# Kernel tuning notes

Hardware: AMD Instinct MI355X
Metric: run time of the kernel (lower is better)

Reference implementation:

```python
import jax, jax.numpy as jnp
import numpy as np
from jax import lax

B, T, L = 16, 256, 1024       # batch, seq_length, input_size
NF = 32                        # num_filters
KS = [3, 5, 7]                 # kernel_sizes
H = 1024                       # feature_size
GRU_IN = NF * len(KS)          # 96


def setup_inputs() -> dict:
    key = jax.random.key(0)
    ks = jax.random.split(key, 20)
    def rn(k, shape, scale):
        return (jax.random.normal(k, shape, dtype=jnp.float32) * scale)
    inp = {
        "x": jax.random.normal(ks[0], (B, T, L), dtype=jnp.float32),
        "conv_w3": rn(ks[1], (NF, 1, 3), (2.0 / 3) ** 0.5),
        "conv_b3": jnp.zeros((NF,), jnp.float32),
        "conv_w5": rn(ks[2], (NF, 1, 5), (2.0 / 5) ** 0.5),
        "conv_b5": jnp.zeros((NF,), jnp.float32),
        "conv_w7": rn(ks[3], (NF, 1, 7), (2.0 / 7) ** 0.5),
        "conv_b7": jnp.zeros((NF,), jnp.float32),
        "gru_w_ih": rn(ks[4], (3 * H, GRU_IN), GRU_IN ** -0.5),
        "gru_w_hh": rn(ks[5], (3 * H, H), H ** -0.5),
        "gru_b_ih": jnp.zeros((3 * H,), jnp.float32),
        "gru_b_hh": jnp.zeros((3 * H,), jnp.float32),
        "attn_w1": rn(ks[6], (H, H), H ** -0.5),
        "attn_b1": jnp.zeros((H,), jnp.float32),
        "attn_w2": rn(ks[7], (1, H), H ** -0.5),
        "attn_b2": jnp.zeros((1,), jnp.float32),
        "fi_w1": rn(ks[8], (H, H), H ** -0.5),
        "fi_b1": jnp.zeros((H,), jnp.float32),
        "fi_w2": rn(ks[9], (H, H), H ** -0.5),
        "fi_b2": jnp.zeros((H,), jnp.float32),
        "lateral": jnp.full((H, H), 0.1, jnp.float32),
    }
    return inp


def _forward(x, conv_w3, conv_b3, conv_w5, conv_b5, conv_w7, conv_b7,
             gru_w_ih, gru_w_hh, gru_b_ih, gru_b_hh,
             attn_w1, attn_b1, attn_w2, attn_b2,
             fi_w1, fi_b1, fi_w2, fi_b2, lateral):
    b, t, l = x.shape
    # --- per-timestep conv branches (no cross-time dependence -> vectorize over B*T) ---
    xt = x.reshape(b * t, 1, l)  # (BT, C=1, L)
    pooled = []
    for w, bias in ((conv_w3, conv_b3), (conv_w5, conv_b5), (conv_w7, conv_b7)):
        y = lax.conv_general_dilated(xt, w, (1,), "SAME",
                                     dimension_numbers=("NCH", "OIH", "NCH"))
        y = jax.nn.relu(y + bias[None, :, None])
        pooled.append(jnp.max(y, axis=-1))  # adaptive_max_pool1d -> (BT, NF)
    feat = jnp.concatenate(pooled, axis=1).reshape(b, t, -1)  # (B, T, 3*NF)

    # --- GRU over time (sequential carry) ---
    gates_x = jnp.einsum("bti,gi->btg", feat, gru_w_ih) + gru_b_ih  # (B,T,3H)

    def step(h, gx):
        gh = h @ gru_w_hh.T + gru_b_hh
        xr, xz, xn = jnp.split(gx, 3, axis=-1)
        hr, hz, hn = jnp.split(gh, 3, axis=-1)
        r = jax.nn.sigmoid(xr + hr)
        z = jax.nn.sigmoid(xz + hz)
        n = jnp.tanh(xn + r * hn)
        h_new = (1.0 - z) * n + z * h
        return h_new, h_new

    h0 = jnp.zeros((b, gru_w_hh.shape[1]), x.dtype)
    _, hs = lax.scan(step, h0, jnp.swapaxes(gates_x, 0, 1))  # (T,B,H)
    hs = jnp.swapaxes(hs, 0, 1)  # (B,T,H)

    # --- attention: per-step softmax over a length-1 axis -> weights are all 1 ---
    scores = jnp.tanh(hs @ attn_w1.T + attn_b1) @ attn_w2.T + attn_b2  # (B,T,1)
    attn = jax.nn.softmax(scores, axis=-1)  # softmax over singleton seq dim -> ones
    attended = hs * attn  # (B,T,H)

    # --- lateral inhibition + feature integration MLP ---
    inhib = attended - jax.nn.relu(jnp.einsum("bth,hf->btf", attended, lateral))
    features = jax.nn.relu(inhib @ fi_w1.T + fi_b1) @ fi_w2.T + fi_b2  # (B,T,H)
    return features, attn[..., 0]  # attention_weights (B,T)


def reference(x, conv_w3, conv_b3, conv_w5, conv_b5, conv_w7, conv_b7,
              gru_w_ih, gru_w_hh, gru_b_ih, gru_b_hh,
              attn_w1, attn_b1, attn_w2, attn_b2,
              fi_w1, fi_b1, fi_w2, fi_b2, lateral):
    return _forward(x, conv_w3, conv_b3, conv_w5, conv_b5, conv_w7, conv_b7,
                    gru_w_ih, gru_w_hh, gru_b_ih, gru_b_hh,
                    attn_w1, attn_b1, attn_w2, attn_b2,
                    fi_w1, fi_b1, fi_w2, fi_b2, lateral)
```

## Files before the change

### kernel.cpp

```cpp
#include <hip/hip_runtime.h>
#include <stdint.h>
#include <stddef.h>

#define B_   16
#define T_   256
#define L_   1024
#define H_   1024
#define G3_  3072
#define KIN_ 96
#define CONVB_ 4096

#define SENT_     0x7FC1
#define SENT_X2_  0x7FC17FC1u

typedef __attribute__((ext_vector_type(8))) __bf16 bf16x8;
typedef __attribute__((ext_vector_type(4))) float  f32x4;
typedef __attribute__((ext_vector_type(4))) int    i32x4;

static __device__ __forceinline__ unsigned short f2bf(float x) {
  unsigned int u = __builtin_bit_cast(unsigned int, x);
  u += 0x7FFFu + ((u >> 16) & 1u);
  return (unsigned short)(u >> 16);
}
static __device__ __forceinline__ float bf2f(unsigned short s) {
  unsigned int u = ((unsigned int)s) << 16;
  return __builtin_bit_cast(float, u);
}
static __device__ __forceinline__ unsigned sentmask(unsigned d) {
  const unsigned x = d ^ SENT_X2_;
  return (x - 0x00010001u) & ~x & 0x80008000u;
}

__global__ __launch_bounds__(256) void prep_conv_kernel(
    const float* __restrict__ x,
    const float* __restrict__ w3, const float* __restrict__ b3,
    const float* __restrict__ w5, const float* __restrict__ b5,
    const float* __restrict__ w7, const float* __restrict__ b7,
    unsigned short* __restrict__ feat,
    const float* __restrict__ whh,  unsigned short* __restrict__ whh_bf,
    const float* __restrict__ wih,  unsigned short* __restrict__ wih_bf,
    const float* __restrict__ fiw1, unsigned short* __restrict__ fiw1_bf,
    const float* __restrict__ fiw2, unsigned short* __restrict__ fiw2_bf,
    const float* __restrict__ lat,  unsigned short* __restrict__ latT_bf,
    unsigned short* __restrict__ hsbuf, float* __restrict__ attn_out) {
  __shared__ float xpad[L_ + 8];
  __shared__ float wlds[96][8];
  __shared__ float blds[96];
  __shared__ float wmax[4][96];
  const int tid = threadIdx.x;

  if (blockIdx.x >= CONVB_) {
    const int N0 = G3_ * H_;
    const int N1 = N0 + G3_ * KIN_;
    const int N2 = N1 + H_ * H_;
    const int N3 = N2 + H_ * H_;
    const int N4 = N3 + H_ * H_;
    const int N5 = N4 + T_ * B_ * H_ / 2;
    const int N6 = N5 + B_ * H_ / 2;
    const int N7 = N6 + B_ * T_;
    int i = (blockIdx.x - CONVB_) * 256 + tid;
    const int stride = (gridDim.x - CONVB_) * 256;
    unsigned int* hs32 = (unsigned int*)hsbuf;
    for (; i < N7; i += stride) {
      if (i < N0)      whh_bf[i] = f2bf(whh[i]);
      else if (i < N1) { const int j = i - N0; wih_bf[j]  = f2bf(wih[j]); }
      else if (i < N2) { const int j = i - N1; fiw1_bf[j] = f2bf(fiw1[j]); }
      else if (i < N3) { const int j = i - N2; fiw2_bf[j] = f2bf(fiw2[j]); }
      else if (i < N4) { const int j = i - N3; const int r = j >> 10, c = j & 1023;
                         latT_bf[(size_t)c * H_ + r] = f2bf(lat[j]); }
      else if (i < N5) { hs32[B_ * H_ / 2 + (i - N4)] = SENT_X2_; }
      else if (i < N6) { hs32[i - N5] = 0u; }
      else             { attn_out[i - N6] = 1.0f; }
    }
    return;
  }

  const int rid = blockIdx.x;
  const int b = rid >> 8;
  const int t = rid & 255;
  const float* xr = x + (size_t)rid * L_;
  for (int off = tid; off < L_; off += 256) xpad[off + 3] = xr[off];
  if (tid < 3) xpad[tid] = 0.f;
  if (tid >= 3 && tid < 8) xpad[L_ + tid] = 0.f;
  if (tid < 96) {
    const int f = tid;
    float wv[8];
#pragma unroll
    for (int k = 0; k < 8; ++k) wv[k] = 0.f;
    float bv;
    if (f < 32)      { for (int k = 0; k < 3; ++k) wv[k + 2] = w3[f * 3 + k]; bv = b3[f]; }
    else if (f < 64) { int ff = f - 32; for (int k = 0; k < 5; ++k) wv[k + 1] = w5[ff * 5 + k]; bv = b5[ff]; }
    else             { int ff = f - 64; for (int k = 0; k < 7; ++k) wv[k] = w7[ff * 7 + k]; bv = b7[ff]; }
#pragma unroll
    for (int k = 0; k < 8; ++k) wlds[f][k] = wv[k];
    blds[f] = bv;
  }
  __syncthreads();
  const int w = tid >> 6, lane = tid & 63;
  const int p0 = w * 256 + lane * 4;
  float xv[10];
#pragma unroll
  for (int i = 0; i < 10; ++i) xv[i] = xpad[p0 + i];
  for (int f = 0; f < 96; ++f) {
    float a0 = 0.f, a1 = 0.f, a2 = 0.f, a3 = 0.f;
#pragma unroll
    for (int k = 0; k < 7; ++k) {
      const float wk = wlds[f][k];
      a0 = fmaf(wk, xv[k],     a0);
      a1 = fmaf(wk, xv[k + 1], a1);
      a2 = fmaf(wk, xv[k + 2], a2);
      a3 = fmaf(wk, xv[k + 3], a3);
    }
    float m = fmaxf(fmaxf(a0, a1), fmaxf(a2, a3));
#pragma unroll
    for (int d = 1; d < 64; d <<= 1) m = fmaxf(m, __shfl_xor(m, d, 64));
    if (lane == 0) wmax[w][f] = m;
  }
  __syncthreads();
  if (tid < 96) {
    float m = fmaxf(fmaxf(wmax[0][tid], wmax[1][tid]),
                    fmaxf(wmax[2][tid], wmax[3][tid]));
    m += blds[tid];
    m = m > 0.f ? m : 0.f;
    feat[(size_t)(t * B_ + b) * KIN_ + tid] = f2bf(m);
  }
}

template <int EP>
__global__ __launch_bounds__(256) void gemm_kernel(
    const unsigned short* __restrict__ A,
    const unsigned short* __restrict__ Bm,
    int M, int N, int K, int lda, int ldb,
    const float* __restrict__ bias,
    float* __restrict__ outF,
    unsigned short* __restrict__ outB) {
  __shared__ __align__(16) unsigned short As[2][128 * 40];
  __shared__ __align__(16) unsigned short Bs[2][128 * 40];
  const int tid = threadIdx.x;
  const int n0 = blockIdx.x * 128;
  const int m0 = blockIdx.y * 128;
  const int w = tid >> 6;
  const int l = tid & 63;
  const int lr = l & 15;
  const int lk = (l >> 4) * 8;
  const int srow = tid >> 2;
  const int skc = (tid & 3) * 8;

  f32x4 acc[2][8];
#pragma unroll
  for (int i = 0; i < 2; ++i)
#pragma unroll
    for (int j = 0; j < 8; ++j) acc[i][j] = (f32x4){0.f, 0.f, 0.f, 0.f};

  const int NK = K >> 5;
  const unsigned short* Aptr  = A  + (size_t)(m0 + srow)      * lda + skc;
  const unsigned short* Aptr2 = A  + (size_t)(m0 + 64 + srow) * lda + skc;
  const unsigned short* Bptr  = Bm + (size_t)(n0 + srow)      * ldb + skc;
  const unsigned short* Bptr2 = Bm + (size_t)(n0 + 64 + srow) * ldb + skc;

  i32x4 ar0 = *(const i32x4*)(Aptr);
  i32x4 ar1 = *(const i32x4*)(Aptr2);
  i32x4 br0 = *(const i32x4*)(Bptr);
  i32x4 br1 = *(const i32x4*)(Bptr2);
  *(i32x4*)&As[0][srow * 40 + skc]        = ar0;
  *(i32x4*)&As[0][(64 + srow) * 40 + skc] = ar1;
  *(i32x4*)&Bs[0][srow * 40 + skc]        = br0;
  *(i32x4*)&Bs[0][(64 + srow) * 40 + skc] = br1;
  __syncthreads();

  for (int kk = 0; kk < NK; ++kk) {
    const int cur = kk & 1;
    if (kk + 1 < NK) {
      const int ko = (kk + 1) << 5;
      ar0 = *(const i32x4*)(Aptr  + ko);
      ar1 = *(const i32x4*)(Aptr2 + ko);
      br0 = *(const i32x4*)(Bptr  + ko);
      br1 = *(const i32x4*)(Bptr2 + ko);
    }
    const bf16x8 a0 = *(const bf16x8*)&As[cur][(w * 32 + lr) * 40 + lk];
    const bf16x8 a1 = *(const bf16x8*)&As[cur][(w * 32 + 16 + lr) * 40 + lk];
#pragma unroll
    for (int nt = 0; nt < 8; ++nt) {
      const bf16x8 bb = *(const bf16x8*)&Bs[cur][(nt * 16 + lr) * 40 + lk];
      acc[0][nt] = __builtin_amdgcn_mfma_f32_16x16x32_bf16(a0, bb, acc[0][nt], 0, 0, 0);
      acc[1][nt] = __builtin_amdgcn_mfma_f32_16x16x32_bf16(a1, bb, acc[1][nt], 0, 0, 0);
    }
    __syncthreads();
    if (kk + 1 < NK) {
      const int nxt = cur ^ 1;
      *(i32x4*)&As[nxt][srow * 40 + skc]        = ar0;
      *(i32x4*)&As[nxt][(64 + srow) * 40 + skc] = ar1;
      *(i32x4*)&Bs[nxt][srow * 40 + skc]        = br0;
      *(i32x4*)&Bs[nxt][(64 + srow) * 40 + skc] = br1;
    }
    __syncthreads();
  }

#pragma unroll
  for (int mt = 0; mt < 2; ++mt) {
#pragma unroll
    for (int nt = 0; nt < 8; ++nt) {
      const f32x4 v = acc[mt][nt];
      const int gcol = n0 + nt * 16 + lr;
#pragma unroll
      for (int e = 0; e < 4; ++e) {
        const int grow = m0 + w * 32 + mt * 16 + (l >> 4) * 4 + e;
        const float val = v[e];
        if (EP == 0) {
          outF[(size_t)grow * N + gcol] = val + bias[gcol];
        } else if (EP == 1) {
          const float hsv = bf2f(A[(size_t)grow * lda + gcol]);
          outB[(size_t)grow * N + gcol] = f2bf(hsv - fmaxf(val, 0.f));
        } else if (EP == 2) {
          outB[(size_t)grow * N + gcol] = f2bf(fmaxf(val + bias[gcol], 0.f));
        } else {
          const int tt = grow >> 4;
          const int bb2 = grow & 15;
          outF[((size_t)bb2 * T_ + tt) * H_ + gcol] = val + bias[gcol];
        }
      }
    }
  }
}

__global__ __launch_bounds__(512, 1) void gru_scan_kernel(
    const unsigned short* __restrict__ Whh,
    const float* __restrict__ gates,
    const float* __restrict__ bhh,
    unsigned short* __restrict__ hs) {
  const int g = blockIdx.x;
  const int tid = threadIdx.x;

  __shared__ float ghp[8][3][16][36];
  const int w = tid >> 6;
  const int l = tid & 63;
  const int lr = l & 15;
  const int lk8 = (l >> 4) * 8;
  const int j0 = g * 32;

  const unsigned short* a00 = Whh + (size_t)(0 * H_ + j0 +      lr) * H_ + w * 128 + lk8;
  const unsigned short* a01 = Whh + (size_t)(0 * H_ + j0 + 16 + lr) * H_ + w * 128 + lk8;
  const unsigned short* a10 = Whh + (size_t)(1 * H_ + j0 +      lr) * H_ + w * 128 + lk8;
  const unsigned short* a11 = Whh + (size_t)(1 * H_ + j0 + 16 + lr) * H_ + w * 128 + lk8;
  const unsigned short* a20 = Whh + (size_t)(2 * H_ + j0 +      lr) * H_ + w * 128 + lk8;
  const unsigned short* a21 = Whh + (size_t)(2 * H_ + j0 + 16 + lr) * H_ + w * 128 + lk8;
  i32x4 q0, q1, q2, q3, q4, q5, q6, q7, q8, q9, q10, q11,
        q12, q13, q14, q15, q16, q17, q18, q19, q20, q21, q22, q23;
  asm volatile(
      "global_load_dwordx4 %0,  %24, off\n\t"
      "global_load_dwordx4 %1,  %24, off offset:64\n\t"
      "global_load_dwordx4 %2,  %24, off offset:128\n\t"
      "global_load_dwordx4 %3,  %24, off offset:192\n\t"
      "global_load_dwordx4 %4,  %25, off\n\t"
      "global_load_dwordx4 %5,  %25, off offset:64\n\t"
      "global_load_dwordx4 %6,  %25, off offset:128\n\t"
      "global_load_dwordx4 %7,  %25, off offset:192\n\t"
      "global_load_dwordx4 %8,  %26, off\n\t"
      "global_load_dwordx4 %9,  %26, off offset:64\n\t"
      "global_load_dwordx4 %10, %26, off offset:128\n\t"
      "global_load_dwordx4 %11, %26, off offset:192\n\t"
      "global_load_dwordx4 %12, %27, off\n\t"
      "global_load_dwordx4 %13, %27, off offset:64\n\t"
      "global_load_dwordx4 %14, %27, off offset:128\n\t"
      "global_load_dwordx4 %15, %27, off offset:192\n\t"
      "global_load_dwordx4 %16, %28, off\n\t"
      "global_load_dwordx4 %17, %28, off offset:64\n\t"
      "global_load_dwordx4 %18, %28, off offset:128\n\t"
      "global_load_dwordx4 %19, %28, off offset:192\n\t"
      "global_load_dwordx4 %20, %29, off\n\t"
      "global_load_dwordx4 %21, %29, off offset:64\n\t"
      "global_load_dwordx4 %22, %29, off offset:128\n\t"
      "global_load_dwordx4 %23, %29, off offset:192\n\t"
      "s_waitcnt vmcnt(0)"
      : "=&v"(q0), "=&v"(q1), "=&v"(q2), "=&v"(q3),
        "=&v"(q4), "=&v"(q5), "=&v"(q6), "=&v"(q7),
        "=&v"(q8), "=&v"(q9), "=&v"(q10), "=&v"(q11),
        "=&v"(q12), "=&v"(q13), "=&v"(q14), "=&v"(q15),
        "=&v"(q16), "=&v"(q17), "=&v"(q18), "=&v"(q19),
        "=&v"(q20), "=&v"(q21), "=&v"(q22), "=&v"(q23)
      : "v"(a00), "v"(a01), "v"(a10), "v"(a11), "v"(a20), "v"(a21));
  bf16x8 wf[24];
  wf[0]  = __builtin_bit_cast(bf16x8, q0);  wf[1]  = __builtin_bit_cast(bf16x8, q1);
  wf[2]  = __builtin_bit_cast(bf16x8, q2);  wf[3]  = __builtin_bit_cast(bf16x8, q3);
  wf[4]  = __builtin_bit_cast(bf16x8, q4);  wf[5]  = __builtin_bit_cast(bf16x8, q5);
  wf[6]  = __builtin_bit_cast(bf16x8, q6);  wf[7]  = __builtin_bit_cast(bf16x8, q7);
  wf[8]  = __builtin_bit_cast(bf16x8, q8);  wf[9]  = __builtin_bit_cast(bf16x8, q9);
  wf[10] = __builtin_bit_cast(bf16x8, q10); wf[11] = __builtin_bit_cast(bf16x8, q11);
  wf[12] = __builtin_bit_cast(bf16x8, q12); wf[13] = __builtin_bit_cast(bf16x8, q13);
  wf[14] = __builtin_bit_cast(bf16x8, q14); wf[15] = __builtin_bit_cast(bf16x8, q15);
  wf[16] = __builtin_bit_cast(bf16x8, q16); wf[17] = __builtin_bit_cast(bf16x8, q17);
  wf[18] = __builtin_bit_cast(bf16x8, q18); wf[19] = __builtin_bit_cast(bf16x8, q19);
  wf[20] = __builtin_bit_cast(bf16x8, q20); wf[21] = __builtin_bit_cast(bf16x8, q21);
  wf[22] = __builtin_bit_cast(bf16x8, q22); wf[23] = __builtin_bit_cast(bf16x8, q23);

  const int jb = tid & 31;
  const int bb = tid >> 5;
  const float bhr = bhh[j0 + jb];
  const float bhz = bhh[H_ + j0 + jb];
  const float bhn = bhh[2 * H_ + j0 + jb];
  float hprev = 0.f;

  for (int t = 0; t < T_; ++t) {
    const size_t grow = ((size_t)t * B_ + bb) * G3_;
    const float gxr = gates[grow + j0 + jb];
    const float gxz = gates[grow + H_ + j0 + jb];
    const float gxn = gates[grow + 2 * H_ + j0 + jb];

    const unsigned short* hp = hs + (size_t)t * (B_ * H_) +
                               (size_t)lr * H_ + w * 128 + lk8;
    i32x4 u0, u1, u2, u3;
    while (true) {
      asm volatile(
          "global_load_dwordx4 %0, %4, off sc0 sc1\n\t"
          "global_load_dwordx4 %1, %4, off offset:64 sc0 sc1\n\t"
          "global_load_dwordx4 %2, %4, off offset:128 sc0 sc1\n\t"
          "global_load_dwordx4 %3, %4, off offset:192 sc0 sc1\n\t"
          "s_waitcnt vmcnt(0)"
          : "=&v"(u0), "=&v"(u1), "=&v"(u2), "=&v"(u3)
          : "v"(hp)
          : "memory");
      const unsigned bad = sentmask(u0[0]) | sentmask(u0[3]) |
                           sentmask(u1[0]) | sentmask(u1[3]) |
                           sentmask(u2[0]) | sentmask(u2[3]) |
                           sentmask(u3[0]) | sentmask(u3[3]);
      if (__ballot(bad == 0) == ~0ull) break;
    }
    const bf16x8 hf0 = __builtin_bit_cast(bf16x8, u0);
    const bf16x8 hf1 = __builtin_bit_cast(bf16x8, u1);
    const bf16x8 hf2 = __builtin_bit_cast(bf16x8, u2);
    const bf16x8 hf3 = __builtin_bit_cast(bf16x8, u3);

    f32x4 C[3][2];
#pragma unroll
    for (int m = 0; m < 3; ++m)
#pragma unroll
      for (int ct = 0; ct < 2; ++ct) C[m][ct] = (f32x4){0.f, 0.f, 0.f, 0.f};
#pragma unroll
    for (int m = 0; m < 3; ++m)
#pragma unroll
      for (int ct = 0; ct < 2; ++ct) {
        C[m][ct] = __builtin_amdgcn_mfma_f32_16x16x32_bf16(wf[(m * 2 + ct) * 4 + 0], hf0, C[m][ct], 0, 0, 0);
        C[m][ct] = __builtin_amdgcn_mfma_f32_16x16x32_bf16(wf[(m * 2 + ct) * 4 + 1], hf1, C[m][ct], 0, 0, 0);
        C[m][ct] = __builtin_amdgcn_mfma_f32_16x16x32_bf16(wf[(m * 2 + ct) * 4 + 2], hf2, C[m][ct], 0, 0, 0);
        C[m][ct] = __builtin_amdgcn_mfma_f32_16x16x32_bf16(wf[(m * 2 + ct) * 4 + 3], hf3, C[m][ct], 0, 0, 0);
      }

    const int rb = (l >> 4) * 4;
#pragma unroll
    for (int m = 0; m < 3; ++m)
#pragma unroll
      for (int ct = 0; ct < 2; ++ct)
#pragma unroll
        for (int e = 0; e < 4; ++e)
          ghp[w][m][lr][ct * 16 + rb + e] = C[m][ct][e];
    __syncthreads();

    float hr = bhr, hz = bhz, hn = bhn;
#pragma unroll
    for (int w2 = 0; w2 < 8; ++w2) {
      hr += ghp[w2][0][bb][jb];
      hz += ghp[w2][1][bb][jb];
      hn += ghp[w2][2][bb][jb];
    }
    const float r = 1.f / (1.f + __expf(-(gxr + hr)));
    const float z = 1.f / (1.f + __expf(-(gxz + hz)));
    const float xn = gxn + r * hn;
    const float n = 2.f / (1.f + __expf(-2.f * xn)) - 1.f;
    const float hnew = (1.f - z) * n + z * hprev;
    hprev = hnew;

    const unsigned hv = (unsigned)f2bf(hnew);
    const int base = l & ~7;
    const unsigned s0 = __shfl(hv, base + 0, 64);
    const unsigned s1 = __shfl(hv, base + 1, 64);
    const unsigned s2 = __shfl(hv, base + 2, 64);
    const unsigned s3 = __shfl(hv, base + 3, 64);
    const unsigned s4 = __shfl(hv, base + 4, 64);
    const unsigned s5 = __shfl(hv, base + 5, 64);
    const unsigned s6 = __shfl(hv, base + 6, 64);
    const unsigned s7 = __shfl(hv, base + 7, 64);
    i32x4 pk;
    pk[0] = (int)(s0 | (s1 << 16));
    pk[1] = (int)(s2 | (s3 << 16));
    pk[2] = (int)(s4 | (s5 << 16));
    pk[3] = (int)(s6 | (s7 << 16));
    if ((l & 7) == 0) {
      unsigned short* sp = hs + ((size_t)(t + 1) * B_ + bb) * H_ + j0 + jb;
      asm volatile("global_store_dwordx4 %0, %1, off sc0 sc1"
                   :: "v"(sp), "v"(pk) : "memory");
    }
    __syncthreads();
  }
}

extern "C" void kernel_launch(void* const* d_in, const int* in_sizes, int n_in,
                              void* d_out, int out_size, void* d_ws, size_t ws_size,
                              hipStream_t stream) {
  (void)in_sizes; (void)n_in; (void)out_size; (void)ws_size;
  const float* x    = (const float*)d_in[0];
  const float* w3   = (const float*)d_in[1];
  const float* b3   = (const float*)d_in[2];
  const float* w5   = (const float*)d_in[3];
  const float* b5   = (const float*)d_in[4];
  const float* w7   = (const float*)d_in[5];
  const float* b7   = (const float*)d_in[6];
  const float* wih  = (const float*)d_in[7];
  const float* whh  = (const float*)d_in[8];
  const float* bih  = (const float*)d_in[9];
  const float* bhh  = (const float*)d_in[10];
  const float* fiw1 = (const float*)d_in[15];
  const float* fib1 = (const float*)d_in[16];
  const float* fiw2 = (const float*)d_in[17];
  const float* fib2 = (const float*)d_in[18];
  const float* lat  = (const float*)d_in[19];

  char* ws = (char*)d_ws;
  size_t off = 0;
  auto alloc = [&](size_t bytes) -> void* {
    void* p = ws + off;
    off += (bytes + 255) & ~(size_t)255;
    return p;
  };
  unsigned short* whh_bf  = (unsigned short*)alloc((size_t)G3_ * H_ * 2);
  unsigned short* wih_bf  = (unsigned short*)alloc((size_t)G3_ * KIN_ * 2);
  unsigned short* latT_bf = (unsigned short*)alloc((size_t)H_ * H_ * 2);
  unsigned short* fiw1_bf = (unsigned short*)alloc((size_t)H_ * H_ * 2);
  unsigned short* fiw2_bf = (unsigned short*)alloc((size_t)H_ * H_ * 2);
  unsigned short* feat_bf = (unsigned short*)alloc((size_t)B_ * T_ * KIN_ * 2);
  float*          gates   = (float*)alloc((size_t)B_ * T_ * G3_ * 4);
  unsigned short* hsbuf   = (unsigned short*)alloc((size_t)(T_ + 1) * B_ * H_ * 2);
  unsigned short* inhib   = (unsigned short*)alloc((size_t)B_ * T_ * H_ * 2);
  unsigned short* y1      = (unsigned short*)alloc((size_t)B_ * T_ * H_ * 2);

  prep_conv_kernel<<<CONVB_ + 2048, 256, 0, stream>>>(
      x, w3, b3, w5, b5, w7, b7, feat_bf,
      whh, whh_bf, wih, wih_bf, fiw1, fiw1_bf, fiw2, fiw2_bf,
      lat, latT_bf, hsbuf, (float*)d_out + (size_t)B_ * T_ * H_);

  {
    dim3 grid(G3_ / 128, (B_ * T_) / 128);
    gemm_kernel<0><<<grid, 256, 0, stream>>>(feat_bf, wih_bf, B_ * T_, G3_, KIN_,
                                             KIN_, KIN_, bih, gates, nullptr);
  }

  gru_scan_kernel<<<32, 512, 0, stream>>>(whh_bf, gates, bhh, hsbuf);

  const unsigned short* hs1 = hsbuf + (size_t)B_ * H_;
  {
    dim3 grid(H_ / 128, (B_ * T_) / 128);
    gemm_kernel<1><<<grid, 256, 0, stream>>>(hs1, latT_bf, B_ * T_, H_, H_,
                                             H_, H_, nullptr, nullptr, inhib);
    gemm_kernel<2><<<grid, 256, 0, stream>>>(inhib, fiw1_bf, B_ * T_, H_, H_,
                                             H_, H_, fib1, nullptr, y1);
    gemm_kernel<3><<<grid, 256, 0, stream>>>(y1, fiw2_bf, B_ * T_, H_, H_,
                                             H_, H_, fib2, (float*)d_out, nullptr);
  }
}
```

Baseline: 907.4 us.

## Halve GRU scan grid by giving each block 64 hidden columns

The persistent GRU scan kernel now launches 16 blocks instead of 32, with each block holding register-resident W_hh slices for 64 hidden units (two 32-column halves) and issuing twice as many MFMAs per step. The aim is to cut the number of blocks that must see each other's hidden-state writes every timestep, which reduces cross-block polling and synchronization latency per step. The cost is double the per-block matrix work and register pressure (48 bf16x8 weight fragments), plus a larger dynamically sized LDS reduction buffer with padded stride 69.

```diff
diff --git a/kernel.cpp b/kernel.cpp
--- a/kernel.cpp
+++ b/kernel.cpp
@@ -228,83 +228,112 @@
     const float* __restrict__ gates,
     const float* __restrict__ bhh,
     unsigned short* __restrict__ hs) {
+  extern __shared__ float ghp[];
   const int g = blockIdx.x;
   const int tid = threadIdx.x;
 
-  __shared__ float ghp[8][3][16][36];
   const int w = tid >> 6;
   const int l = tid & 63;
   const int lr = l & 15;
   const int lk8 = (l >> 4) * 8;
-  const int j0 = g * 32;
-
-  const unsigned short* a00 = Whh + (size_t)(0 * H_ + j0 +      lr) * H_ + w * 128 + lk8;
-  const unsigned short* a01 = Whh + (size_t)(0 * H_ + j0 + 16 + lr) * H_ + w * 128 + lk8;
-  const unsigned short* a10 = Whh + (size_t)(1 * H_ + j0 +      lr) * H_ + w * 128 + lk8;
-  const unsigned short* a11 = Whh + (size_t)(1 * H_ + j0 + 16 + lr) * H_ + w * 128 + lk8;
-  const unsigned short* a20 = Whh + (size_t)(2 * H_ + j0 +      lr) * H_ + w * 128 + lk8;
-  const unsigned short* a21 = Whh + (size_t)(2 * H_ + j0 + 16 + lr) * H_ + w * 128 + lk8;
-  i32x4 q0, q1, q2, q3, q4, q5, q6, q7, q8, q9, q10, q11,
-        q12, q13, q14, q15, q16, q17, q18, q19, q20, q21, q22, q23;
-  asm volatile(
-      "global_load_dwordx4 %0,  %24, off\n\t"
-      "global_load_dwordx4 %1,  %24, off offset:64\n\t"
-      "global_load_dwordx4 %2,  %24, off offset:128\n\t"
-      "global_load_dwordx4 %3,  %24, off offset:192\n\t"
-      "global_load_dwordx4 %4,  %25, off\n\t"
-      "global_load_dwordx4 %5,  %25, off offset:64\n\t"
-      "global_load_dwordx4 %6,  %25, off offset:128\n\t"
-      "global_load_dwordx4 %7,  %25, off offset:192\n\t"
-      "global_load_dwordx4 %8,  %26, off\n\t"
-      "global_load_dwordx4 %9,  %26, off offset:64\n\t"
-      "global_load_dwordx4 %10, %26, off offset:128\n\t"
-      "global_load_dwordx4 %11, %26, off offset:192\n\t"
-      "global_load_dwordx4 %12, %27, off\n\t"
-      "global_load_dwordx4 %13, %27, off offset:64\n\t"
-      "global_load_dwordx4 %14, %27, off offset:128\n\t"
-      "global_load_dwordx4 %15, %27, off offset:192\n\t"
-      "global_load_dwordx4 %16, %28, off\n\t"
-      "global_load_dwordx4 %17, %28, off offset:64\n\t"
-      "global_load_dwordx4 %18, %28, off offset:128\n\t"
-      "global_load_dwordx4 %19, %28, off offset:192\n\t"
-      "global_load_dwordx4 %20, %29, off\n\t"
-      "global_load_dwordx4 %21, %29, off offset:64\n\t"
-      "global_load_dwordx4 %22, %29, off offset:128\n\t"
-      "global_load_dwordx4 %23, %29, off offset:192\n\t"
-      "s_waitcnt vmcnt(0)"
-      : "=&v"(q0), "=&v"(q1), "=&v"(q2), "=&v"(q3),
-        "=&v"(q4), "=&v"(q5), "=&v"(q6), "=&v"(q7),
-        "=&v"(q8), "=&v"(q9), "=&v"(q10), "=&v"(q11),
-        "=&v"(q12), "=&v"(q13), "=&v"(q14), "=&v"(q15),
-        "=&v"(q16), "=&v"(q17), "=&v"(q18), "=&v"(q19),
-        "=&v"(q20), "=&v"(q21), "=&v"(q22), "=&v"(q23)
-      : "v"(a00), "v"(a01), "v"(a10), "v"(a11), "v"(a20), "v"(a21));
-  bf16x8 wf[24];
-  wf[0]  = __builtin_bit_cast(bf16x8, q0);  wf[1]  = __builtin_bit_cast(bf16x8, q1);
-  wf[2]  = __builtin_bit_cast(bf16x8, q2);  wf[3]  = __builtin_bit_cast(bf16x8, q3);
-  wf[4]  = __builtin_bit_cast(bf16x8, q4);  wf[5]  = __builtin_bit_cast(bf16x8, q5);
-  wf[6]  = __builtin_bit_cast(bf16x8, q6);  wf[7]  = __builtin_bit_cast(bf16x8, q7);
-  wf[8]  = __builtin_bit_cast(bf16x8, q8);  wf[9]  = __builtin_bit_cast(bf16x8, q9);
-  wf[10] = __builtin_bit_cast(bf16x8, q10); wf[11] = __builtin_bit_cast(bf16x8, q11);
-  wf[12] = __builtin_bit_cast(bf16x8, q12); wf[13] = __builtin_bit_cast(bf16x8, q13);
-  wf[14] = __builtin_bit_cast(bf16x8, q14); wf[15] = __builtin_bit_cast(bf16x8, q15);
-  wf[16] = __builtin_bit_cast(bf16x8, q16); wf[17] = __builtin_bit_cast(bf16x8, q17);
-  wf[18] = __builtin_bit_cast(bf16x8, q18); wf[19] = __builtin_bit_cast(bf16x8, q19);
-  wf[20] = __builtin_bit_cast(bf16x8, q20); wf[21] = __builtin_bit_cast(bf16x8, q21);
-  wf[22] = __builtin_bit_cast(bf16x8, q22); wf[23] = __builtin_bit_cast(bf16x8, q23);
+  const int j0 = g * 64;
+
+#define GHP(W, M, BB, CC) ghp[(((W) * 3 + (M)) * 16 + (BB)) * 69 + (CC)]
+
+  bf16x8 wf[48];
+#pragma unroll
+  for (int half = 0; half < 2; ++half) {
+    const int jh = j0 + half * 32;
+    const unsigned short* a00 = Whh + (size_t)(0 * H_ + jh +      lr) * H_ + w * 128 + lk8;
+    const unsigned short* a01 = Whh + (size_t)(0 * H_ + jh + 16 + lr) * H_ + w * 128 + lk8;
+    const unsigned short* a10 = Whh + (size_t)(1 * H_ + jh +      lr) * H_ + w * 128 + lk8;
+    const unsigned short* a11 = Whh + (size_t)(1 * H_ + jh + 16 + lr) * H_ + w * 128 + lk8;
+    const unsigned short* a20 = Whh + (size_t)(2 * H_ + jh +      lr) * H_ + w * 128 + lk8;
+    const unsigned short* a21 = Whh + (size_t)(2 * H_ + jh + 16 + lr) * H_ + w * 128 + lk8;
+    i32x4 q0, q1, q2, q3, q4, q5, q6, q7, q8, q9, q10, q11,
+          q12, q13, q14, q15, q16, q17, q18, q19, q20, q21, q22, q23;
+    asm volatile(
+        "global_load_dwordx4 %0,  %24, off\n\t"
+        "global_load_dwordx4 %1,  %24, off offset:64\n\t"
+        "global_load_dwordx4 %2,  %24, off offset:128\n\t"
+        "global_load_dwordx4 %3,  %24, off offset:192\n\t"
+        "global_load_dwordx4 %4,  %25, off\n\t"
+        "global_load_dwordx4 %5,  %25, off offset:64\n\t"
+        "global_load_dwordx4 %6,  %25, off offset:128\n\t"
+        "global_load_dwordx4 %7,  %25, off offset:192\n\t"
+        "global_load_dwordx4 %8,  %26, off\n\t"
+        "global_load_dwordx4 %9,  %26, off offset:64\n\t"
+        "global_load_dwordx4 %10, %26, off offset:128\n\t"
+        "global_load_dwordx4 %11, %26, off offset:192\n\t"
+        "global_load_dwordx4 %12, %27, off\n\t"
+        "global_load_dwordx4 %13, %27, off offset:64\n\t"
+        "global_load_dwordx4 %14, %27, off offset:128\n\t"
+        "global_load_dwordx4 %15, %27, off offset:192\n\t"
+        "global_load_dwordx4 %16, %28, off\n\t"
+        "global_load_dwordx4 %17, %28, off offset:64\n\t"
+        "global_load_dwordx4 %18, %28, off offset:128\n\t"
+        "global_load_dwordx4 %19, %28, off offset:192\n\t"
+        "global_load_dwordx4 %20, %29, off\n\t"
+        "global_load_dwordx4 %21, %29, off offset:64\n\t"
+        "global_load_dwordx4 %22, %29, off offset:128\n\t"
+        "global_load_dwordx4 %23, %29, off offset:192\n\t"
+        "s_waitcnt vmcnt(0)"
+        : "=&v"(q0), "=&v"(q1), "=&v"(q2), "=&v"(q3),
+          "=&v"(q4), "=&v"(q5), "=&v"(q6), "=&v"(q7),
+          "=&v"(q8), "=&v"(q9), "=&v"(q10), "=&v"(q11),
+          "=&v"(q12), "=&v"(q13), "=&v"(q14), "=&v"(q15),
+          "=&v"(q16), "=&v"(q17), "=&v"(q18), "=&v"(q19),
+          "=&v"(q20), "=&v"(q21), "=&v"(q22), "=&v"(q23)
+        : "v"(a00), "v"(a01), "v"(a10), "v"(a11), "v"(a20), "v"(a21));
+    const int b0 = half * 2;
+    wf[(0 * 4 + b0 + 0) * 4 + 0] = __builtin_bit_cast(bf16x8, q0);
+    wf[(0 * 4 + b0 + 0) * 4 + 1] = __builtin_bit_cast(bf16x8, q1);
+    wf[(0 * 4 + b0 + 0) * 4 + 2] = __builtin_bit_cast(bf16x8, q2);
+    wf[(0 * 4 + b0 + 0) * 4 + 3] = __builtin_bit_cast(bf16x8, q3);
+    wf[(0 * 4 + b0 + 1) * 4 + 0] = __builtin_bit_cast(bf16x8, q4);
+    wf[(0 * 4 + b0 + 1) * 4 + 1] = __builtin_bit_cast(bf16x8, q5);
+    wf[(0 * 4 + b0 + 1) * 4 + 2] = __builtin_bit_cast(bf16x8, q6);
+    wf[(0 * 4 + b0 + 1) * 4 + 3] = __builtin_bit_cast(bf16x8, q7);
+    wf[(1 * 4 + b0 + 0) * 4 + 0] = __builtin_bit_cast(bf16x8, q8);
+    wf[(1 * 4 + b0 + 0) * 4 + 1] = __builtin_bit_cast(bf16x8, q9);
+    wf[(1 * 4 + b0 + 0) * 4 + 2] = __builtin_bit_cast(bf16x8, q10);
+    wf[(1 * 4 + b0 + 0) * 4 + 3] = __builtin_bit_cast(bf16x8, q11);
+    wf[(1 * 4 + b0 + 1) * 4 + 0] = __builtin_bit_cast(bf16x8, q12);
+    wf[(1 * 4 + b0 + 1) * 4 + 1] = __builtin_bit_cast(bf16x8, q13);
+    wf[(1 * 4 + b0 + 1) * 4 + 2] = __builtin_bit_cast(bf16x8, q14);
+    wf[(1 * 4 + b0 + 1) * 4 + 3] = __builtin_bit_cast(bf16x8, q15);
+    wf[(2 * 4 + b0 + 0) * 4 + 0] = __builtin_bit_cast(bf16x8, q16);
+    wf[(2 * 4 + b0 + 0) * 4 + 1] = __builtin_bit_cast(bf16x8, q17);
+    wf[(2 * 4 + b0 + 0) * 4 + 2] = __builtin_bit_cast(bf16x8, q18);
+    wf[(2 * 4 + b0 + 0) * 4 + 3] = __builtin_bit_cast(bf16x8, q19);
+    wf[(2 * 4 + b0 + 1) * 4 + 0] = __builtin_bit_cast(bf16x8, q20);
+    wf[(2 * 4 + b0 + 1) * 4 + 1] = __builtin_bit_cast(bf16x8, q21);
+    wf[(2 * 4 + b0 + 1) * 4 + 2] = __builtin_bit_cast(bf16x8, q22);
+    wf[(2 * 4 + b0 + 1) * 4 + 3] = __builtin_bit_cast(bf16x8, q23);
+  }
 
   const int jb = tid & 31;
   const int bb = tid >> 5;
-  const float bhr = bhh[j0 + jb];
-  const float bhz = bhh[H_ + j0 + jb];
-  const float bhn = bhh[2 * H_ + j0 + jb];
-  float hprev = 0.f;
+  float bhg[2][3], hprev[2];
+#pragma unroll
+  for (int half = 0; half < 2; ++half) {
+    const int jc = j0 + half * 32 + jb;
+    bhg[half][0] = bhh[jc];
+    bhg[half][1] = bhh[H_ + jc];
+    bhg[half][2] = bhh[2 * H_ + jc];
+    hprev[half] = 0.f;
+  }
 
   for (int t = 0; t < T_; ++t) {
     const size_t grow = ((size_t)t * B_ + bb) * G3_;
-    const float gxr = gates[grow + j0 + jb];
-    const float gxz = gates[grow + H_ + j0 + jb];
-    const float gxn = gates[grow + 2 * H_ + j0 + jb];
+    float gx[2][3];
+#pragma unroll
+    for (int half = 0; half < 2; ++half) {
+      const int jc = j0 + half * 32 + jb;
+      gx[half][0] = gates[grow + jc];
+      gx[half][1] = gates[grow + H_ + jc];
+      gx[half][2] = gates[grow + 2 * H_ + jc];
+    }
 
     const unsigned short* hp = hs + (size_t)t * (B_ * H_) +
                                (size_t)lr * H_ + w * 128 + lk8;
@@ -330,67 +359,73 @@
     const bf16x8 hf2 = __builtin_bit_cast(bf16x8, u2);
     const bf16x8 hf3 = __builtin_bit_cast(bf16x8, u3);
 
-    f32x4 C[3][2];
+    f32x4 C[3][4];
 #pragma unroll
     for (int m = 0; m < 3; ++m)
 #pragma unroll
-      for (int ct = 0; ct < 2; ++ct) C[m][ct] = (f32x4){0.f, 0.f, 0.f, 0.f};
+      for (int ct = 0; ct < 4; ++ct) C[m][ct] = (f32x4){0.f, 0.f, 0.f, 0.f};
 #pragma unroll
     for (int m = 0; m < 3; ++m)
 #pragma unroll
-      for (int ct = 0; ct < 2; ++ct) {
-        C[m][ct] = __builtin_amdgcn_mfma_f32_16x16x32_bf16(wf[(m * 2 + ct) * 4 + 0], hf0, C[m][ct], 0, 0, 0);
-        C[m][ct] = __builtin_amdgcn_mfma_f32_16x16x32_bf16(wf[(m * 2 + ct) * 4 + 1], hf1, C[m][ct], 0, 0, 0);
-        C[m][ct] = __builtin_amdgcn_mfma_f32_16x16x32_bf16(wf[(m * 2 + ct) * 4 + 2], hf2, C[m][ct], 0, 0, 0);
-        C[m][ct] = __builtin_amdgcn_mfma_f32_16x16x32_bf16(wf[(m * 2 + ct) * 4 + 3], hf3, C[m][ct], 0, 0, 0);
+      for (int ct = 0; ct < 4; ++ct) {
+        C[m][ct] = __builtin_amdgcn_mfma_f32_16x16x32_bf16(wf[(m * 4 + ct) * 4 + 0], hf0, C[m][ct], 0, 0, 0);
+        C[m][ct] = __builtin_amdgcn_mfma_f32_16x16x32_bf16(wf[(m * 4 + ct) * 4 + 1], hf1, C[m][ct], 0, 0, 0);
+        C[m][ct] = __builtin_amdgcn_mfma_f32_16x16x32_bf16(wf[(m * 4 + ct) * 4 + 2], hf2, C[m][ct], 0, 0, 0);
+        C[m][ct] = __builtin_amdgcn_mfma_f32_16x16x32_bf16(wf[(m * 4 + ct) * 4 + 3], hf3, C[m][ct], 0, 0, 0);
       }
 
     const int rb = (l >> 4) * 4;
 #pragma unroll
     for (int m = 0; m < 3; ++m)
 #pragma unroll
-      for (int ct = 0; ct < 2; ++ct)
+      for (int ct = 0; ct < 4; ++ct)
 #pragma unroll
         for (int e = 0; e < 4; ++e)
-          ghp[w][m][lr][ct * 16 + rb + e] = C[m][ct][e];
+          GHP(w, m, lr, ct * 16 + rb + e) = C[m][ct][e];
     __syncthreads();
 
-    float hr = bhr, hz = bhz, hn = bhn;
-#pragma unroll
-    for (int w2 = 0; w2 < 8; ++w2) {
-      hr += ghp[w2][0][bb][jb];
-      hz += ghp[w2][1][bb][jb];
-      hn += ghp[w2][2][bb][jb];
-    }
-    const float r = 1.f / (1.f + __expf(-(gxr + hr)));
-    const float z = 1.f / (1.f + __expf(-(gxz + hz)));
-    const float xn = gxn + r * hn;
-    const float n = 2.f / (1.f + __expf(-2.f * xn)) - 1.f;
-    const float hnew = (1.f - z) * n + z * hprev;
-    hprev = hnew;
-
-    const unsigned hv = (unsigned)f2bf(hnew);
-    const int base = l & ~7;
-    const unsigned s0 = __shfl(hv, base + 0, 64);
-    const unsigned s1 = __shfl(hv, base + 1, 64);
-    const unsigned s2 = __shfl(hv, base + 2, 64);
-    const unsigned s3 = __shfl(hv, base + 3, 64);
-    const unsigned s4 = __shfl(hv, base + 4, 64);
-    const unsigned s5 = __shfl(hv, base + 5, 64);
-    const unsigned s6 = __shfl(hv, base + 6, 64);
-    const unsigned s7 = __shfl(hv, base + 7, 64);
-    i32x4 pk;
-    pk[0] = (int)(s0 | (s1 << 16));
-    pk[1] = (int)(s2 | (s3 << 16));
-    pk[2] = (int)(s4 | (s5 << 16));
-    pk[3] = (int)(s6 | (s7 << 16));
-    if ((l & 7) == 0) {
-      unsigned short* sp = hs + ((size_t)(t + 1) * B_ + bb) * H_ + j0 + jb;
-      asm volatile("global_store_dwordx4 %0, %1, off sc0 sc1"
-                   :: "v"(sp), "v"(pk) : "memory");
+#pragma unroll
+    for (int half = 0; half < 2; ++half) {
+      const int jc32 = half * 32 + jb;
+      float hr = bhg[half][0], hz = bhg[half][1], hn = bhg[half][2];
+#pragma unroll
+      for (int w2 = 0; w2 < 8; ++w2) {
+        hr += GHP(w2, 0, bb, jc32);
+        hz += GHP(w2, 1, bb, jc32);
+        hn += GHP(w2, 2, bb, jc32);
+      }
+      const float r = 1.f / (1.f + __expf(-(gx[half][0] + hr)));
+      const float z = 1.f / (1.f + __expf(-(gx[half][1] + hz)));
+      const float xn = gx[half][2] + r * hn;
+      const float n = 2.f / (1.f + __expf(-2.f * xn)) - 1.f;
+      const float hnew = (1.f - z) * n + z * hprev[half];
+      hprev[half] = hnew;
+
+      const unsigned hv = (unsigned)f2bf(hnew);
+      const int base = l & ~7;
+      const unsigned s0 = __shfl(hv, base + 0, 64);
+      const unsigned s1 = __shfl(hv, base + 1, 64);
+      const unsigned s2 = __shfl(hv, base + 2, 64);
+      const unsigned s3 = __shfl(hv, base + 3, 64);
+      const unsigned s4 = __shfl(hv, base + 4, 64);
+      const unsigned s5 = __shfl(hv, base + 5, 64);
+      const unsigned s6 = __shfl(hv, base + 6, 64);
+      const unsigned s7 = __shfl(hv, base + 7, 64);
+      i32x4 pk;
+      pk[0] = (int)(s0 | (s1 << 16));
+      pk[1] = (int)(s2 | (s3 << 16));
+      pk[2] = (int)(s4 | (s5 << 16));
+      pk[3] = (int)(s6 | (s7 << 16));
+      if ((l & 7) == 0) {
+        unsigned short* sp = hs + ((size_t)(t + 1) * B_ + bb) * H_ +
+                             j0 + half * 32 + jb;
+        asm volatile("global_store_dwordx4 %0, %1, off sc0 sc1"
+                     :: "v"(sp), "v"(pk) : "memory");
+      }
     }
     __syncthreads();
   }
+#undef GHP
 }
 
 extern "C" void kernel_launch(void* const* d_in, const int* in_sizes, int n_in,
@@ -443,7 +478,8 @@
                                              KIN_, KIN_, bih, gates, nullptr);
   }
 
-  gru_scan_kernel<<<32, 512, 0, stream>>>(whh_bf, gates, bhh, hsbuf);
+  const size_t scan_lds = (size_t)8 * 3 * 16 * 69 * 4;
+  gru_scan_kernel<<<16, 512, scan_lds, stream>>>(whh_bf, gates, bhh, hsbuf);
 
   const unsigned short* hs1 = hsbuf + (size_t)B_ * H_;
   {
```

After: 1.825 ms. +101.1%, slower.
